# Kernel optimization log

Measured on AMD Instinct MI355X. Metric: run time of the kernel, lower is better.

Reference implementation:

```python
import jax, jax.numpy as jnp
import numpy as np

N_TOKENS = 3
EMBED = 10
RNN = 10
N_LABELS = 3
B = 16384
T = 99
EPS = 1e-7  # keras CategoricalCrossentropy clip epsilon


def setup_inputs() -> dict:
    key = jax.random.key(0)
    ks = jax.random.split(key, 8)
    token_ids = jax.random.randint(ks[0], (B, T), 0, N_TOKENS, dtype=jnp.int32)
    label_ids = jax.random.randint(ks[1], (B, T), 0, N_LABELS)
    labels = jax.nn.one_hot(label_ids, N_LABELS, dtype=jnp.float32)
    mask = jnp.ones((B, T), dtype=bool)  # accepted by call() but unused, kept for signature fidelity
    emb_table = jax.random.normal(ks[2], (N_TOKENS, EMBED), jnp.float32) * 0.05
    W = jax.random.normal(ks[3], (EMBED, RNN), jnp.float32) / np.sqrt(EMBED)
    U = jax.random.normal(ks[4], (RNN, RNN), jnp.float32) / np.sqrt(RNN)
    b = jnp.zeros((RNN,), jnp.float32)
    Wo = jax.random.normal(ks[5], (RNN, N_LABELS), jnp.float32) / np.sqrt(RNN)
    bo = jnp.zeros((N_LABELS,), jnp.float32)
    return dict(token_ids=token_ids, labels=labels, mask=mask,
                emb_table=emb_table, W=W, U=U, b=b, Wo=Wo, bo=bo)


def reference(token_ids, labels, mask, emb_table, W, U, b, Wo, bo):
    # Embedding lookup (mask_zero=True -> token 0 is a masked step)
    emb = emb_table[token_ids]                      # [B, T, E]
    step_mask = (token_ids != 0)                    # [B, T]

    def step(h, inp):
        x_t, m_t = inp                              # [B, E], [B]
        h_new = jnp.tanh(x_t @ W + h @ U + b)       # SimpleRNN cell
        # Keras masking: masked timesteps carry previous state/output
        h = jnp.where(m_t[:, None], h_new, h)
        return h, h

    h0 = jnp.zeros((token_ids.shape[0], W.shape[1]), emb.dtype)
    _, states_tb = jax.lax.scan(step, h0, (emb.transpose(1, 0, 2), step_mask.T))
    states = states_tb.transpose(1, 0, 2)           # [B, T, R]

    probs = jax.nn.softmax(states @ Wo + bo, axis=-1)   # Dense(softmax) -> [B, T, L]
    probs_c = jnp.clip(probs, EPS, 1.0)
    loss = jnp.mean(-jnp.sum(labels * jnp.log(probs_c), axis=-1))
    accuracy = jnp.mean((jnp.argmax(probs, axis=-1) == jnp.argmax(labels, axis=-1)).astype(jnp.float32))
    return states, probs, accuracy, loss
```

## Files before the change

kernel.cpp:

```cpp
#include <hip/hip_runtime.h>
#include <math.h>

#define BB 16384
#define TT 99
#define RR 10
#define LL 3
#define TILE 33
#define RPW 16
#define WPB 4

#define QPB(v, Q) __int_as_float(__builtin_amdgcn_mov_dpp(                    \
    __float_as_int(v), (Q) * 0x55, 0xF, 0xF, true))

__device__ __forceinline__ float fast_tanh(float x) {
    float e = __expf(2.0f * x);
    return fmaf(-2.0f, __builtin_amdgcn_rcpf(e + 1.0f), 1.0f);
}

__global__ __launch_bounds__(256, 1)
void rnn_fused_kernel(const int* __restrict__ tok_ids,
                      const float* __restrict__ labels,
                      const float* __restrict__ emb,
                      const float* __restrict__ W,
                      const float* __restrict__ U,
                      const float* __restrict__ bvec,
                      const float* __restrict__ Wo,
                      const float* __restrict__ bo,
                      float* __restrict__ states_out,
                      float* __restrict__ probs_out,
                      float* __restrict__ ws)
{
    __shared__ __align__(16) float          s_st[WPB][RPW * TILE * RR];
    __shared__                unsigned char s_code[WPB][RPW * 100];

    const int tid = threadIdx.x;
    const int w   = tid >> 6;
    const int l   = tid & 63;
    const int r4  = l >> 2;
    const int q   = l & 3;
    const int rowbase = blockIdx.x * (WPB * RPW) + w * RPW;

#pragma unroll 1
    for (int g = 0; g < 5; ++g) {
#pragma unroll
        for (int u = 0; u < 5; ++u) {
            const int p = l + 64 * (g * 5 + u);
            if (p < RPW * TT) {
                const size_t gi = (size_t)rowbase * TT + p;
                const int   tk  = tok_ids[gi];
                const float la1 = labels[gi * LL + 1];
                const float la2 = labels[gi * LL + 2];
                const int   y   = (la1 > 0.5f) ? 1 : ((la2 > 0.5f) ? 2 : 0);
                const int   r   = p / TT;
                s_code[w][r * 100 + (p - r * TT)] = (unsigned char)((tk << 2) | y);
            }
        }
    }

    const int uA = q;
    const int uB = 4 + q;
    const int uC = (q < 2) ? 8 + q : q;
    float UA[RR], UB[RR], UC[RR];
    float cA1 = bvec[uA], cA2 = cA1;
    float cB1 = bvec[uB], cB2 = cB1;
    float cC1 = bvec[uC], cC2 = cC1;
#pragma unroll
    for (int i = 0; i < RR; ++i) {
        UA[i] = U[i * RR + uA];
        UB[i] = U[i * RR + uB];
        UC[i] = U[i * RR + uC];
        const float wA = W[i * RR + uA];
        const float wB = W[i * RR + uB];
        const float wC = W[i * RR + uC];
        const float e1 = emb[RR + i];
        const float e2 = emb[2 * RR + i];
        cA1 = fmaf(e1, wA, cA1); cA2 = fmaf(e2, wA, cA2);
        cB1 = fmaf(e1, wB, cB1); cB2 = fmaf(e2, wB, cB2);
        cC1 = fmaf(e1, wC, cC1); cC2 = fmaf(e2, wC, cC2);
    }

    float hoA = 0.0f, hoB = 0.0f, hoC = 0.0f;
    float loss = 0.0f;
    int   corr = 0;
    int code = (int)s_code[w][r4 * 100];

#pragma unroll 1
    for (int k = 0; k < 3; ++k) {
#pragma unroll 1
        for (int tt = 0; tt < TILE; ++tt) {
            const int t   = k * TILE + tt;
            const int cur = code;
            const int tn  = (t + 1 < TT) ? t + 1 : t;
            code = (int)s_code[w][r4 * 100 + tn];
            const int sel = cur >> 2;

            float h[RR];
            h[0] = QPB(hoA, 0); h[1] = QPB(hoA, 1);
            h[2] = QPB(hoA, 2); h[3] = QPB(hoA, 3);
            h[4] = QPB(hoB, 0); h[5] = QPB(hoB, 1);
            h[6] = QPB(hoB, 2); h[7] = QPB(hoB, 3);
            h[8] = QPB(hoC, 0); h[9] = QPB(hoC, 1);

            const bool is1 = (sel == 1);
            float aA = is1 ? cA1 : cA2;
            float aB = is1 ? cB1 : cB2;
            float aC = is1 ? cC1 : cC2;
#pragma unroll
            for (int i = 0; i < RR; ++i) {
                aA = fmaf(h[i], UA[i], aA);
                aB = fmaf(h[i], UB[i], aB);
                aC = fmaf(h[i], UC[i], aC);
            }
            const float hnA = fast_tanh(aA);
            const float hnB = fast_tanh(aB);
            const float hnC = fast_tanh(aC);
            if (sel != 0) { hoA = hnA; hoB = hnB; hoC = hnC; }

            float* sp = &s_st[w][(r4 * TILE + tt) * RR];
            sp[q]     = hoA;
            sp[4 + q] = hoB;
            if (q < 2) sp[8 + q] = hoC;
        }

#pragma unroll
        for (int i = 0; i < 42; ++i) {
            const int p = l + 64 * i;
            if (p < RPW * TILE * RR / 2) {
                const int r = p / 165;
                const int m = p - r * 165;
                const float2 v = *reinterpret_cast<const float2*>(
                    &s_st[w][r * (TILE * RR) + 2 * m]);
                *reinterpret_cast<float2*>(
                    &states_out[(size_t)(rowbase + r) * (TT * RR)
                                + (size_t)k * (TILE * RR) + 2 * m]) = v;
            }
        }

#pragma unroll
        for (int i = 0; i < 9; ++i) {
            const int p = l + 64 * i;
            if (p < RPW * TILE) {
                const int r  = p / TILE;
                const int t2 = p - r * TILE;
                const size_t idx = (size_t)(rowbase + r) * TT + k * TILE + t2;

                const float* hp = &s_st[w][(r * TILE + t2) * RR];
                float l0 = bo[0], l1 = bo[1], l2 = bo[2];
#pragma unroll
                for (int j = 0; j < RR; ++j) {
                    const float hj = hp[j];
                    l0 = fmaf(hj, Wo[j * LL + 0], l0);
                    l1 = fmaf(hj, Wo[j * LL + 1], l1);
                    l2 = fmaf(hj, Wo[j * LL + 2], l2);
                }
                const float e0 = __expf(l0), e1 = __expf(l1), e2 = __expf(l2);
                const float S  = e0 + e1 + e2;
                const float rs = __builtin_amdgcn_rcpf(S);
                probs_out[idx * LL + 0] = e0 * rs;
                probs_out[idx * LL + 1] = e1 * rs;
                probs_out[idx * LL + 2] = e2 * rs;

                const int y = (int)s_code[w][r * 100 + k * TILE + t2] & 3;

                const float ly = (y == 0) ? l0 : ((y == 1) ? l1 : l2);
                loss += fminf(__logf(S) - ly, 16.11809565f);

                int ap = 0; float pm = l0;
                if (l1 > pm) { ap = 1; pm = l1; }
                if (l2 > pm) { ap = 2; }
                corr += (ap == y) ? 1 : 0;
            }
        }
    }

    float ls = loss, cs = (float)corr;
#pragma unroll
    for (int off = 32; off > 0; off >>= 1) {
        ls += __shfl_down(ls, off, 64);
        cs += __shfl_down(cs, off, 64);
    }
    if (l == 0) {
        const int wid = blockIdx.x * WPB + w;
        ws[wid]        = ls;
        ws[1024 + wid] = cs;
    }
}

__global__ __launch_bounds__(256)
void finalize_kernel(const float* __restrict__ ws, float* __restrict__ out_tail)
{
    __shared__ float sl[4], sc[4];
    const int t = threadIdx.x;
    float ls = 0.0f, cs = 0.0f;
#pragma unroll
    for (int i = 0; i < 4; ++i) {
        ls += ws[t + 256 * i];
        cs += ws[1024 + t + 256 * i];
    }
#pragma unroll
    for (int off = 32; off > 0; off >>= 1) {
        ls += __shfl_down(ls, off, 64);
        cs += __shfl_down(cs, off, 64);
    }
    if ((t & 63) == 0) { sl[t >> 6] = ls; sc[t >> 6] = cs; }
    __syncthreads();
    if (t == 0) {
        const float L = sl[0] + sl[1] + sl[2] + sl[3];
        const float C = sc[0] + sc[1] + sc[2] + sc[3];
        const float inv = 1.0f / (float)((size_t)BB * TT);
        out_tail[0] = C * inv;
        out_tail[1] = L * inv;
    }
}

extern "C" void kernel_launch(void* const* d_in, const int* in_sizes, int n_in,
                              void* d_out, int out_size, void* d_ws, size_t ws_size,
                              hipStream_t stream)
{
    const int*   tok    = (const int*)  d_in[0];
    const float* labels = (const float*)d_in[1];
    const float* emb = (const float*)d_in[3];
    const float* W   = (const float*)d_in[4];
    const float* U   = (const float*)d_in[5];
    const float* bv  = (const float*)d_in[6];
    const float* Wo  = (const float*)d_in[7];
    const float* bo  = (const float*)d_in[8];

    float* out    = (float*)d_out;
    float* states = out;
    float* probs  = out + (size_t)BB * TT * RR;
    float* tail   = out + (size_t)BB * TT * (RR + LL);
    float* ws     = (float*)d_ws;

    rnn_fused_kernel<<<BB / (WPB * RPW), 256, 0, stream>>>(
        tok, labels, emb, W, U, bv, Wo, bo, states, probs, ws);
    finalize_kernel<<<1, 256, 0, stream>>>(ws, tail);
}
```

Baseline: 52.22 us.

## Split each RNN row across 8 lanes with DPP row-mirror broadcast and 8 rows per wave

Each batch row is now handled by 8 lanes instead of 4, and each wave covers 8 rows instead of 16. The kernel launches twice as many blocks, and launch bounds allow two blocks per CU. Hidden-state exchange uses quad-perm DPP plus a row-mirror DPP, and the recurrent dot product is split into two accumulator chains to shorten the dependency chain. The sequential latency per step drops and more waves can be resident, but each wave does less useful work, and partial-sum slots grow to 2048 per array.

```diff
diff --git a/kernel.cpp b/kernel.cpp
--- a/kernel.cpp
+++ b/kernel.cpp
@@ -6,18 +6,20 @@
 #define RR 10
 #define LL 3
 #define TILE 33
-#define RPW 16
+#define RPW 8
 #define WPB 4
 
-#define QPB(v, Q) __int_as_float(__builtin_amdgcn_mov_dpp(                    \
-    __float_as_int(v), (Q) * 0x55, 0xF, 0xF, true))
+#define QP(v, j) __int_as_float(__builtin_amdgcn_mov_dpp(                     \
+    __float_as_int(v), (j) * 0x55, 0xF, 0xF, true))
+#define HMIR(v)  __int_as_float(__builtin_amdgcn_mov_dpp(                     \
+    __float_as_int(v), 0x141, 0xF, 0xF, true))
 
 __device__ __forceinline__ float fast_tanh(float x) {
     float e = __expf(2.0f * x);
     return fmaf(-2.0f, __builtin_amdgcn_rcpf(e + 1.0f), 1.0f);
 }
 
-__global__ __launch_bounds__(256, 1)
+__global__ __launch_bounds__(256, 2)
 void rnn_fused_kernel(const int* __restrict__ tok_ids,
                       const float* __restrict__ labels,
                       const float* __restrict__ emb,
@@ -36,53 +38,58 @@
     const int tid = threadIdx.x;
     const int w   = tid >> 6;
     const int l   = tid & 63;
-    const int r4  = l >> 2;
-    const int q   = l & 3;
+    const int r8  = l >> 3;
+    const int g   = l & 7;
     const int rowbase = blockIdx.x * (WPB * RPW) + w * RPW;
 
 #pragma unroll 1
-    for (int g = 0; g < 5; ++g) {
-#pragma unroll
-        for (int u = 0; u < 5; ++u) {
-            const int p = l + 64 * (g * 5 + u);
-            if (p < RPW * TT) {
-                const size_t gi = (size_t)rowbase * TT + p;
-                const int   tk  = tok_ids[gi];
-                const float la1 = labels[gi * LL + 1];
-                const float la2 = labels[gi * LL + 2];
-                const int   y   = (la1 > 0.5f) ? 1 : ((la2 > 0.5f) ? 2 : 0);
-                const int   r   = p / TT;
-                s_code[w][r * 100 + (p - r * TT)] = (unsigned char)((tk << 2) | y);
-            }
-        }
-    }
-
-    const int uA = q;
-    const int uB = 4 + q;
-    const int uC = (q < 2) ? 8 + q : q;
-    float UA[RR], UB[RR], UC[RR];
-    float cA1 = bvec[uA], cA2 = cA1;
-    float cB1 = bvec[uB], cB2 = cB1;
-    float cC1 = bvec[uC], cC2 = cC1;
+    for (int i = 0; i < 13; ++i) {
+        const int p = l + 64 * i;
+        if (p < RPW * TT) {
+            const size_t gi = (size_t)rowbase * TT + p;
+            const int   tk  = tok_ids[gi];
+            const float la1 = labels[gi * LL + 1];
+            const float la2 = labels[gi * LL + 2];
+            const int   y   = (la1 > 0.5f) ? 1 : ((la2 > 0.5f) ? 2 : 0);
+            const int   r   = p / TT;
+            s_code[w][r * 100 + (p - r * TT)] = (unsigned char)((tk << 2) | y);
+        }
+    }
+
+    const int qpar = g >> 2;
+    int ord[8];
+#pragma unroll
+    for (int j = 0; j < 4; ++j) {
+        ord[j]     = qpar ? 4 + j : j;
+        ord[4 + j] = qpar ? 3 - j : 7 - j;
+    }
+    const int jA = g;
+    const int jB = ((g & 3) < 2) ? 8 + (g & 3) : 8;
+
+    float UA[RR], UB[RR];
+#pragma unroll
+    for (int k2 = 0; k2 < 8; ++k2) {
+        UA[k2] = U[ord[k2] * RR + jA];
+        UB[k2] = U[ord[k2] * RR + jB];
+    }
+    UA[8] = U[8 * RR + jA]; UA[9] = U[9 * RR + jA];
+    UB[8] = U[8 * RR + jB]; UB[9] = U[9 * RR + jB];
+
+    float cA1 = bvec[jA], cA2 = cA1, cB1 = bvec[jB], cB2 = cB1;
 #pragma unroll
     for (int i = 0; i < RR; ++i) {
-        UA[i] = U[i * RR + uA];
-        UB[i] = U[i * RR + uB];
-        UC[i] = U[i * RR + uC];
-        const float wA = W[i * RR + uA];
-        const float wB = W[i * RR + uB];
-        const float wC = W[i * RR + uC];
         const float e1 = emb[RR + i];
         const float e2 = emb[2 * RR + i];
+        const float wA = W[i * RR + jA];
+        const float wB = W[i * RR + jB];
         cA1 = fmaf(e1, wA, cA1); cA2 = fmaf(e2, wA, cA2);
         cB1 = fmaf(e1, wB, cB1); cB2 = fmaf(e2, wB, cB2);
-        cC1 = fmaf(e1, wC, cC1); cC2 = fmaf(e2, wC, cC2);
-    }
-
-    float hoA = 0.0f, hoB = 0.0f, hoC = 0.0f;
+    }
+
+    float hoA = 0.0f, hoB = 0.0f;
     float loss = 0.0f;
     int   corr = 0;
-    int code = (int)s_code[w][r4 * 100];
+    int code = (int)s_code[w][r8 * 100];
 
 #pragma unroll 1
     for (int k = 0; k < 3; ++k) {
@@ -91,41 +98,40 @@
             const int t   = k * TILE + tt;
             const int cur = code;
             const int tn  = (t + 1 < TT) ? t + 1 : t;
-            code = (int)s_code[w][r4 * 100 + tn];
+            code = (int)s_code[w][r8 * 100 + tn];
             const int sel = cur >> 2;
 
-            float h[RR];
-            h[0] = QPB(hoA, 0); h[1] = QPB(hoA, 1);
-            h[2] = QPB(hoA, 2); h[3] = QPB(hoA, 3);
-            h[4] = QPB(hoB, 0); h[5] = QPB(hoB, 1);
-            h[6] = QPB(hoB, 2); h[7] = QPB(hoB, 3);
-            h[8] = QPB(hoC, 0); h[9] = QPB(hoC, 1);
+            float hg[RR];
+            hg[0] = QP(hoA, 0); hg[1] = QP(hoA, 1);
+            hg[2] = QP(hoA, 2); hg[3] = QP(hoA, 3);
+            const float mr = HMIR(hoA);
+            hg[4] = QP(mr, 0);  hg[5] = QP(mr, 1);
+            hg[6] = QP(mr, 2);  hg[7] = QP(mr, 3);
+            hg[8] = QP(hoB, 0); hg[9] = QP(hoB, 1);
 
             const bool is1 = (sel == 1);
-            float aA = is1 ? cA1 : cA2;
-            float aB = is1 ? cB1 : cB2;
-            float aC = is1 ? cC1 : cC2;
-#pragma unroll
-            for (int i = 0; i < RR; ++i) {
-                aA = fmaf(h[i], UA[i], aA);
-                aB = fmaf(h[i], UB[i], aB);
-                aC = fmaf(h[i], UC[i], aC);
+            float aA0 = is1 ? cA1 : cA2, aB0 = is1 ? cB1 : cB2;
+            float aA1 = 0.0f, aB1 = 0.0f;
+#pragma unroll
+            for (int i = 0; i < 5; ++i) {
+                aA0 = fmaf(hg[i],     UA[i],     aA0);
+                aA1 = fmaf(hg[5 + i], UA[5 + i], aA1);
+                aB0 = fmaf(hg[i],     UB[i],     aB0);
+                aB1 = fmaf(hg[5 + i], UB[5 + i], aB1);
             }
-            const float hnA = fast_tanh(aA);
-            const float hnB = fast_tanh(aB);
-            const float hnC = fast_tanh(aC);
-            if (sel != 0) { hoA = hnA; hoB = hnB; hoC = hnC; }
-
-            float* sp = &s_st[w][(r4 * TILE + tt) * RR];
-            sp[q]     = hoA;
-            sp[4 + q] = hoB;
-            if (q < 2) sp[8 + q] = hoC;
-        }
-
-#pragma unroll
-        for (int i = 0; i < 42; ++i) {
+            const float hnA = fast_tanh(aA0 + aA1);
+            const float hnB = fast_tanh(aB0 + aB1);
+            if (sel != 0) { hoA = hnA; hoB = hnB; }
+
+            float* sp = &s_st[w][(r8 * TILE + tt) * RR];
+            sp[g] = hoA;
+            if (g < 2) sp[8 + g] = hoB;
+        }
+
+#pragma unroll 1
+        for (int i = 0; i < 21; ++i) {
             const int p = l + 64 * i;
-            if (p < RPW * TILE * RR / 2) {
+            if (p < 1320) {
                 const int r = p / 165;
                 const int m = p - r * 165;
                 const float2 v = *reinterpret_cast<const float2*>(
@@ -136,8 +142,8 @@
             }
         }
 
-#pragma unroll
-        for (int i = 0; i < 9; ++i) {
+#pragma unroll 1
+        for (int i = 0; i < 5; ++i) {
             const int p = l + 64 * i;
             if (p < RPW * TILE) {
                 const int r  = p / TILE;
@@ -145,13 +151,18 @@
                 const size_t idx = (size_t)(rowbase + r) * TT + k * TILE + t2;
 
                 const float* hp = &s_st[w][(r * TILE + t2) * RR];
+                float h0[RR];
+#pragma unroll
+                for (int j = 0; j < RR; j += 2) {
+                    const float2 v = *reinterpret_cast<const float2*>(hp + j);
+                    h0[j] = v.x; h0[j + 1] = v.y;
+                }
                 float l0 = bo[0], l1 = bo[1], l2 = bo[2];
 #pragma unroll
                 for (int j = 0; j < RR; ++j) {
-                    const float hj = hp[j];
-                    l0 = fmaf(hj, Wo[j * LL + 0], l0);
-                    l1 = fmaf(hj, Wo[j * LL + 1], l1);
-                    l2 = fmaf(hj, Wo[j * LL + 2], l2);
+                    l0 = fmaf(h0[j], Wo[j * LL + 0], l0);
+                    l1 = fmaf(h0[j], Wo[j * LL + 1], l1);
+                    l2 = fmaf(h0[j], Wo[j * LL + 2], l2);
                 }
                 const float e0 = __expf(l0), e1 = __expf(l1), e2 = __expf(l2);
                 const float S  = e0 + e1 + e2;
@@ -182,7 +193,7 @@
     if (l == 0) {
         const int wid = blockIdx.x * WPB + w;
         ws[wid]        = ls;
-        ws[1024 + wid] = cs;
+        ws[2048 + wid] = cs;
     }
 }
 
@@ -193,9 +204,9 @@
     const int t = threadIdx.x;
     float ls = 0.0f, cs = 0.0f;
 #pragma unroll
-    for (int i = 0; i < 4; ++i) {
+    for (int i = 0; i < 8; ++i) {
         ls += ws[t + 256 * i];
-        cs += ws[1024 + t + 256 * i];
+        cs += ws[2048 + t + 256 * i];
     }
 #pragma unroll
     for (int off = 32; off > 0; off >>= 1) {
```

New measurement: 51.11 us. 1.02x faster.
